# Optimization experiments

Measured on AMD Instinct MI355X. Metric: run time of the kernel, lower is better.

The kernel has to match this reference:

```python
import jax, jax.numpy as jnp
import numpy as np

EPS = 1e-12  # matches torch F.normalize eps


def setup_inputs() -> dict:
    key = jax.random.key(0)
    k_x, k_w, k_b, k_c, k_f = jax.random.split(key, 5)
    N, C, H, W = 32, 128, 64, 64
    K = 64
    x = jax.random.normal(k_x, (N, C, H, W), dtype=jnp.float32)
    conv_w = jax.random.normal(k_w, (K, C), dtype=jnp.float32) * 0.05  # 1x1 conv weight [K,C,1,1] squeezed
    conv_b = jax.random.normal(k_b, (K,), dtype=jnp.float32) * 0.05
    centroids = jax.random.uniform(k_c, (K, C), dtype=jnp.float32)
    fc_w = jax.random.normal(k_f, (1, K), dtype=jnp.float32) * 0.1  # nn.Linear(K,1,bias=False).weight
    return {"x": x, "conv_w": conv_w, "conv_b": conv_b, "centroids": centroids, "fc_w": fc_w}


def _l2norm(v, axis):
    return v / jnp.maximum(jnp.linalg.norm(v, axis=axis, keepdims=True), EPS)


def reference(x, conv_w, conv_b, centroids, fc_w):
    N, C, H, W = x.shape
    K = conv_w.shape[0]
    # descriptor-wise L2 normalize over channel dim
    x = _l2norm(x, axis=1)
    xf = x.reshape(N, C, H * W)                                   # [N,C,S]
    # 1x1 conv == per-pixel linear over channels
    logits = jnp.einsum('kc,ncs->nks', conv_w, xf) + conv_b[None, :, None]
    a = jax.nn.softmax(logits, axis=1)                            # [N,K,S] soft assignment
    # VLAD: sum_s a[n,k,s] * (x[n,:,s] - centroids[k,:]), loop-free
    vlad = jnp.einsum('nks,ncs->nkc', a, xf) \
           - a.sum(axis=-1)[..., None] * centroids[None, :, :]    # [N,K,C]
    # intra-normalization over descriptor dim
    vlad = _l2norm(vlad, axis=2)
    # lastfc: [N,C,K] @ [K] -> [N,C]
    out = jnp.einsum('nkc,k->nc', vlad, fc_w[0])
    return out
```

## Files before the change

### kernel.cpp

```cpp
#include <hip/hip_runtime.h>
#include <math.h>

#define Nn 32
#define Cc 128
#define Ss 4096
#define Kk 64
#define NCHUNK 16
#define SCHUNK (Ss / NCHUNK)
#define ST 64
#define NSUB (SCHUNK / ST)
#define BLK 256

#define XCS 72
#define XTS 136
#define LKS 68
#define AS  72
#define RS  17

typedef __attribute__((ext_vector_type(8))) short short8;
typedef __attribute__((ext_vector_type(4))) float float4v;

__device__ __forceinline__ unsigned f2bf(float f) {
    unsigned u = __builtin_bit_cast(unsigned, f);
    return (u + 0x7fffu + ((u >> 16) & 1u)) >> 16;
}
__device__ __forceinline__ unsigned pack2(float a, float b) {
    return f2bf(a) | (f2bf(b) << 16);
}

__global__ __launch_bounds__(BLK, 2) void netvlad_main(
    const float* __restrict__ x,
    const float* __restrict__ conv_w,
    const float* __restrict__ conv_b,
    float* __restrict__ vlad,
    float* __restrict__ asum)
{
    __shared__ __align__(16) unsigned short xC[Cc * XCS];
    __shared__ __align__(16) float Lbuf[ST * LKS];
    __shared__ __align__(16) unsigned short aB[Kk * AS];
    __shared__ float red[ST * RS];
    __shared__ float invn[ST];
    unsigned short* xT = (unsigned short*)Lbuf;

    const int t    = threadIdx.x;
    const int n    = blockIdx.y;
    const int w    = t >> 6;
    const int l    = t & 63;
    const int m    = l & 15;
    const int quad = l >> 4;
    const int p    = t >> 2;
    const int ii   = t & 3;

    short8 wfrag[4];
    {
        const float* wr_ = conv_w + (16 * w + m) * Cc;
#pragma unroll
        for (int ks = 0; ks < 4; ++ks) {
            float4 wa = *(const float4*)(wr_ + 32 * ks + 8 * quad);
            float4 wb = *(const float4*)(wr_ + 32 * ks + 8 * quad + 4);
            union { short8 s8; unsigned u[4]; } W_;
            W_.u[0] = pack2(wa.x, wa.y);
            W_.u[1] = pack2(wa.z, wa.w);
            W_.u[2] = pack2(wb.x, wb.y);
            W_.u[3] = pack2(wb.z, wb.w);
            wfrag[ks] = W_.s8;
        }
    }
    float bias_r[4];
#pragma unroll
    for (int r = 0; r < 4; ++r) bias_r[r] = conv_b[16 * w + 4 * quad + r];

    float4v acc[8];
#pragma unroll
    for (int nt = 0; nt < 8; ++nt) acc[nt] = (float4v){0.f, 0.f, 0.f, 0.f};
    float asum_part[16];
#pragma unroll
    for (int j = 0; j < 16; ++j) asum_part[j] = 0.f;

    const float* xn = x + (size_t)n * Cc * Ss;

    for (int sub = 0; sub < NSUB; ++sub) {
        const int s0 = blockIdx.x * SCHUNK + sub * ST;
        __syncthreads();

        {
            float sp0 = 0.f, sp1 = 0.f, sp2 = 0.f, sp3 = 0.f;
            const int sq = (t & 15) << 2;
#pragma unroll
            for (int r = 0; r < 8; ++r) {
                int c = (t >> 4) + 16 * r;
                float4 v = *(const float4*)(xn + (size_t)c * Ss + s0 + sq);
                sp0 += v.x * v.x; sp1 += v.y * v.y;
                sp2 += v.z * v.z; sp3 += v.w * v.w;
                uint2 pk = make_uint2(pack2(v.x, v.y), pack2(v.z, v.w));
                *(uint2*)&xC[c * XCS + sq] = pk;
            }
            red[(sq + 0) * RS + (t >> 4)] = sp0;
            red[(sq + 1) * RS + (t >> 4)] = sp1;
            red[(sq + 2) * RS + (t >> 4)] = sp2;
            red[(sq + 3) * RS + (t >> 4)] = sp3;
        }
        __syncthreads();

        if (t < ST) {
            float tot = 0.f;
#pragma unroll
            for (int i = 0; i < 16; ++i) tot += red[t * RS + i];
            invn[t] = 1.0f / fmaxf(sqrtf(tot), 1e-12f);
        }
        {
            int s = t & 63, oct0 = t >> 6;
#pragma unroll
            for (int q = 0; q < 4; ++q) {
                int oct = oct0 + 4 * q;
                uint4 dd;
                dd.x = (unsigned)xC[(8 * oct + 0) * XCS + s] | ((unsigned)xC[(8 * oct + 1) * XCS + s] << 16);
                dd.y = (unsigned)xC[(8 * oct + 2) * XCS + s] | ((unsigned)xC[(8 * oct + 3) * XCS + s] << 16);
                dd.z = (unsigned)xC[(8 * oct + 4) * XCS + s] | ((unsigned)xC[(8 * oct + 5) * XCS + s] << 16);
                dd.w = (unsigned)xC[(8 * oct + 6) * XCS + s] | ((unsigned)xC[(8 * oct + 7) * XCS + s] << 16);
                *(uint4*)&xT[s * XTS + 8 * oct] = dd;
            }
        }
        __syncthreads();

        float4v Lr[4];
#pragma unroll
        for (int nt = 0; nt < 4; ++nt) Lr[nt] = (float4v){0.f, 0.f, 0.f, 0.f};
#pragma unroll
        for (int nt = 0; nt < 4; ++nt) {
#pragma unroll
            for (int ks = 0; ks < 4; ++ks) {
                short8 b = *(const short8*)&xT[(16 * nt + m) * XTS + 32 * ks + 8 * quad];
                Lr[nt] = __builtin_amdgcn_mfma_f32_16x16x32_bf16(wfrag[ks], b, Lr[nt], 0, 0, 0);
            }
        }
        __syncthreads();

#pragma unroll
        for (int nt = 0; nt < 4; ++nt) {
            float iv = invn[16 * nt + m];
            float4 o;
            o.x = Lr[nt].x * iv + bias_r[0];
            o.y = Lr[nt].y * iv + bias_r[1];
            o.z = Lr[nt].z * iv + bias_r[2];
            o.w = Lr[nt].w * iv + bias_r[3];
            *(float4*)&Lbuf[(16 * nt + m) * LKS + 16 * w + 4 * quad] = o;
        }
        __syncthreads();

        {
            float lv[16];
#pragma unroll
            for (int j = 0; j < 16; ++j) lv[j] = Lbuf[p * LKS + ii + 4 * j];
            float mx = lv[0];
#pragma unroll
            for (int j = 1; j < 16; ++j) mx = fmaxf(mx, lv[j]);
            mx = fmaxf(mx, __shfl_xor(mx, 1));
            mx = fmaxf(mx, __shfl_xor(mx, 2));
            float e[16];
            float lsum = 0.f;
#pragma unroll
            for (int j = 0; j < 16; ++j) { e[j] = __expf(lv[j] - mx); lsum += e[j]; }
            lsum += __shfl_xor(lsum, 1);
            lsum += __shfl_xor(lsum, 2);
            float itot = 1.0f / lsum;
            float sca  = itot * invn[p];
#pragma unroll
            for (int j = 0; j < 16; ++j) {
                float av = e[j] * itot;
                asum_part[j] += av;
                aB[(ii + 4 * j) * AS + p] = (unsigned short)f2bf(e[j] * sca);
            }
        }
        __syncthreads();

#pragma unroll
        for (int ks = 0; ks < 2; ++ks) {
            short8 af = *(const short8*)&aB[(16 * w + m) * AS + 32 * ks + 8 * quad];
#pragma unroll
            for (int nt = 0; nt < 8; ++nt) {
                short8 bf_ = *(const short8*)&xC[(16 * nt + m) * XCS + 32 * ks + 8 * quad];
                acc[nt] = __builtin_amdgcn_mfma_f32_16x16x32_bf16(af, bf_, acc[nt], 0, 0, 0);
            }
        }
    }

    float* vb = vlad + ((size_t)n * Kk + 16 * w + 4 * quad) * Cc + m;
#pragma unroll
    for (int nt = 0; nt < 8; ++nt) {
        atomicAdd(vb + 0 * Cc + 16 * nt, acc[nt].x);
        atomicAdd(vb + 1 * Cc + 16 * nt, acc[nt].y);
        atomicAdd(vb + 2 * Cc + 16 * nt, acc[nt].z);
        atomicAdd(vb + 3 * Cc + 16 * nt, acc[nt].w);
    }

    __syncthreads();
#pragma unroll
    for (int j = 0; j < 16; ++j) Lbuf[p * LKS + ii + 4 * j] = asum_part[j];
    __syncthreads();
    if (t < Kk) {
        float s_ = 0.f;
        for (int p2 = 0; p2 < ST; ++p2) s_ += Lbuf[p2 * LKS + t];
        atomicAdd(&asum[n * Kk + t], s_);
    }
}

__global__ __launch_bounds__(256) void netvlad_final(
    const float* __restrict__ vlad, const float* __restrict__ asum,
    const float* __restrict__ centroids, const float* __restrict__ fc_w,
    float* __restrict__ out)
{
    __shared__ float scale_s[Kk];
    __shared__ float asum_s[Kk];
    __shared__ float red2[Kk][4];

    const int n = blockIdx.x;
    const int t = threadIdx.x;
    const int k = t >> 2;
    const int q = t & 3;

    const float* vr = vlad + ((size_t)n * Kk + k) * Cc + q * 32;
    const float* cr = centroids + k * Cc + q * 32;
    const float  as = asum[n * Kk + k];

    float ssq = 0.f;
#pragma unroll
    for (int i = 0; i < 8; ++i) {
        float4 v4 = *(const float4*)(vr + 4 * i);
        float4 c4 = *(const float4*)(cr + 4 * i);
        float d0 = v4.x - as * c4.x;
        float d1 = v4.y - as * c4.y;
        float d2 = v4.z - as * c4.z;
        float d3 = v4.w - as * c4.w;
        ssq += d0 * d0 + d1 * d1 + d2 * d2 + d3 * d3;
    }
    red2[k][q] = ssq;
    __syncthreads();
    if (q == 0) {
        float tot = red2[k][0] + red2[k][1] + red2[k][2] + red2[k][3];
        scale_s[k] = fc_w[k] / fmaxf(sqrtf(tot), 1e-12f);
        asum_s[k]  = as;
    }
    __syncthreads();

    if (t < Cc) {
        const int c = t;
        const float* vbp = vlad + (size_t)n * Kk * Cc + c;
        float o = 0.f;
#pragma unroll 8
        for (int k2 = 0; k2 < Kk; ++k2)
            o += scale_s[k2] * (vbp[k2 * Cc] - asum_s[k2] * centroids[k2 * Cc + c]);
        out[n * Cc + c] = o;
    }
}

extern "C" void kernel_launch(void* const* d_in, const int* in_sizes, int n_in,
                              void* d_out, int out_size, void* d_ws, size_t ws_size,
                              hipStream_t stream) {
    (void)in_sizes; (void)n_in; (void)out_size; (void)ws_size;
    const float* x         = (const float*)d_in[0];
    const float* conv_w    = (const float*)d_in[1];
    const float* conv_b    = (const float*)d_in[2];
    const float* centroids = (const float*)d_in[3];
    const float* fc_w      = (const float*)d_in[4];
    float* out = (float*)d_out;

    float* vlad = (float*)d_ws;
    float* asum = vlad + (size_t)Nn * Kk * Cc;
    size_t zero_bytes = ((size_t)Nn * Kk * Cc + (size_t)Nn * Kk) * sizeof(float);
    hipMemsetAsync(d_ws, 0, zero_bytes, stream);

    dim3 grid(NCHUNK, Nn);
    netvlad_main<<<grid, BLK, 0, stream>>>(x, conv_w, conv_b, vlad, asum);
    netvlad_final<<<Nn, 256, 0, stream>>>(vlad, asum, centroids, fc_w, out);
}
```

Before: 119.3 us.

## Keep conv logits in registers and do softmax per wave without LDS round trip

Each wave now computes all 64 clusters for its own 16 pixels, holding all four weight k-tiles in registers. The softmax is then done directly on the MFMA accumulators with cross-lane shuffles, which removes the Lbuf spill and two barriers per subtile. It also adds a faster transpose using 32-bit LDS reads, computes the per-pixel norm with shuffles, and reduces asum with shuffles. NCHUNK is doubled and the occupancy hint is raised to 3, at the cost of more weight registers and more atomics.

```diff
diff --git a/kernel.cpp b/kernel.cpp
--- a/kernel.cpp
+++ b/kernel.cpp
@@ -5,7 +5,7 @@
 #define Cc 128
 #define Ss 4096
 #define Kk 64
-#define NCHUNK 16
+#define NCHUNK 32
 #define SCHUNK (Ss / NCHUNK)
 #define ST 64
 #define NSUB (SCHUNK / ST)
@@ -13,9 +13,8 @@
 
 #define XCS 72
 #define XTS 136
-#define LKS 68
 #define AS  72
-#define RS  17
+#define RSS 68
 
 typedef __attribute__((ext_vector_type(8))) short short8;
 typedef __attribute__((ext_vector_type(4))) float float4v;
@@ -28,7 +27,7 @@
     return f2bf(a) | (f2bf(b) << 16);
 }
 
-__global__ __launch_bounds__(BLK, 2) void netvlad_main(
+__global__ __launch_bounds__(BLK, 3) void netvlad_main(
     const float* __restrict__ x,
     const float* __restrict__ conv_w,
     const float* __restrict__ conv_b,
@@ -36,24 +35,25 @@
     float* __restrict__ asum)
 {
     __shared__ __align__(16) unsigned short xC[Cc * XCS];
-    __shared__ __align__(16) float Lbuf[ST * LKS];
+    __shared__ __align__(16) unsigned short xT[ST * XTS];
     __shared__ __align__(16) unsigned short aB[Kk * AS];
-    __shared__ float red[ST * RS];
-    __shared__ float invn[ST];
-    unsigned short* xT = (unsigned short*)Lbuf;
+    __shared__ __align__(16) float red[16 * RSS];
+    __shared__ float bias_lds[Kk];
+    float* asumLDS = red;
 
     const int t    = threadIdx.x;
     const int n    = blockIdx.y;
     const int w    = t >> 6;
-    const int l    = t & 63;
-    const int m    = l & 15;
-    const int quad = l >> 4;
-    const int p    = t >> 2;
-    const int ii   = t & 3;
-
-    short8 wfrag[4];
-    {
-        const float* wr_ = conv_w + (16 * w + m) * Cc;
+    const int m    = t & 15;
+    const int quad = (t >> 4) & 3;
+    const int sw   = 16 * w + m;
+
+    if (t < Kk) bias_lds[t] = conv_b[t];
+
+    short8 wfrag[4][4];
+#pragma unroll
+    for (int kt = 0; kt < 4; ++kt) {
+        const float* wr_ = conv_w + (16 * kt + m) * Cc;
 #pragma unroll
         for (int ks = 0; ks < 4; ++ks) {
             float4 wa = *(const float4*)(wr_ + 32 * ks + 8 * quad);
@@ -63,12 +63,9 @@
             W_.u[1] = pack2(wa.z, wa.w);
             W_.u[2] = pack2(wb.x, wb.y);
             W_.u[3] = pack2(wb.z, wb.w);
-            wfrag[ks] = W_.s8;
-        }
-    }
-    float bias_r[4];
-#pragma unroll
-    for (int r = 0; r < 4; ++r) bias_r[r] = conv_b[16 * w + 4 * quad + r];
+            wfrag[kt][ks] = W_.s8;
+        }
+    }
 
     float4v acc[8];
 #pragma unroll
@@ -84,92 +81,90 @@
         __syncthreads();
 
         {
+            const int g  = t >> 4;
+            const int sq = (t & 15) << 2;
             float sp0 = 0.f, sp1 = 0.f, sp2 = 0.f, sp3 = 0.f;
-            const int sq = (t & 15) << 2;
 #pragma unroll
             for (int r = 0; r < 8; ++r) {
-                int c = (t >> 4) + 16 * r;
+                int c = g + 16 * r;
                 float4 v = *(const float4*)(xn + (size_t)c * Ss + s0 + sq);
                 sp0 += v.x * v.x; sp1 += v.y * v.y;
                 sp2 += v.z * v.z; sp3 += v.w * v.w;
                 uint2 pk = make_uint2(pack2(v.x, v.y), pack2(v.z, v.w));
                 *(uint2*)&xC[c * XCS + sq] = pk;
             }
-            red[(sq + 0) * RS + (t >> 4)] = sp0;
-            red[(sq + 1) * RS + (t >> 4)] = sp1;
-            red[(sq + 2) * RS + (t >> 4)] = sp2;
-            red[(sq + 3) * RS + (t >> 4)] = sp3;
-        }
-        __syncthreads();
-
-        if (t < ST) {
-            float tot = 0.f;
-#pragma unroll
-            for (int i = 0; i < 16; ++i) tot += red[t * RS + i];
-            invn[t] = 1.0f / fmaxf(sqrtf(tot), 1e-12f);
-        }
+            *(float4*)&red[g * RSS + sq] = make_float4(sp0, sp1, sp2, sp3);
+        }
+        __syncthreads();
+
+#pragma unroll
+        for (int pass = 0; pass < 2; ++pass) {
+            int oct = (t >> 5) + 8 * pass;
+            int sp2_ = t & 31;
+            unsigned r_[8];
+#pragma unroll
+            for (int j = 0; j < 8; ++j)
+                r_[j] = *(const unsigned*)&xC[(8 * oct + j) * XCS + 2 * sp2_];
+            uint4 lo, hi;
+            lo.x = (r_[0] & 0xffffu) | (r_[1] << 16);
+            lo.y = (r_[2] & 0xffffu) | (r_[3] << 16);
+            lo.z = (r_[4] & 0xffffu) | (r_[5] << 16);
+            lo.w = (r_[6] & 0xffffu) | (r_[7] << 16);
+            hi.x = (r_[0] >> 16) | (r_[1] & 0xffff0000u);
+            hi.y = (r_[2] >> 16) | (r_[3] & 0xffff0000u);
+            hi.z = (r_[4] >> 16) | (r_[5] & 0xffff0000u);
+            hi.w = (r_[6] >> 16) | (r_[7] & 0xffff0000u);
+            *(uint4*)&xT[(2 * sp2_ + 0) * XTS + 8 * oct] = lo;
+            *(uint4*)&xT[(2 * sp2_ + 1) * XTS + 8 * oct] = hi;
+        }
+
+        float pr = red[(4 * quad + 0) * RSS + sw] + red[(4 * quad + 1) * RSS + sw]
+                 + red[(4 * quad + 2) * RSS + sw] + red[(4 * quad + 3) * RSS + sw];
+        pr += __shfl_xor(pr, 16);
+        pr += __shfl_xor(pr, 32);
+        float invn = 1.0f / fmaxf(sqrtf(pr), 1e-12f);
+        __syncthreads();
+
+        float4v Lr[4];
+#pragma unroll
+        for (int kt = 0; kt < 4; ++kt) Lr[kt] = (float4v){0.f, 0.f, 0.f, 0.f};
+#pragma unroll
+        for (int ks = 0; ks < 4; ++ks) {
+            short8 b = *(const short8*)&xT[sw * XTS + 32 * ks + 8 * quad];
+#pragma unroll
+            for (int kt = 0; kt < 4; ++kt)
+                Lr[kt] = __builtin_amdgcn_mfma_f32_16x16x32_bf16(wfrag[kt][ks], b, Lr[kt], 0, 0, 0);
+        }
+
         {
-            int s = t & 63, oct0 = t >> 6;
-#pragma unroll
-            for (int q = 0; q < 4; ++q) {
-                int oct = oct0 + 4 * q;
-                uint4 dd;
-                dd.x = (unsigned)xC[(8 * oct + 0) * XCS + s] | ((unsigned)xC[(8 * oct + 1) * XCS + s] << 16);
-                dd.y = (unsigned)xC[(8 * oct + 2) * XCS + s] | ((unsigned)xC[(8 * oct + 3) * XCS + s] << 16);
-                dd.z = (unsigned)xC[(8 * oct + 4) * XCS + s] | ((unsigned)xC[(8 * oct + 5) * XCS + s] << 16);
-                dd.w = (unsigned)xC[(8 * oct + 6) * XCS + s] | ((unsigned)xC[(8 * oct + 7) * XCS + s] << 16);
-                *(uint4*)&xT[s * XTS + 8 * oct] = dd;
-            }
-        }
-        __syncthreads();
-
-        float4v Lr[4];
-#pragma unroll
-        for (int nt = 0; nt < 4; ++nt) Lr[nt] = (float4v){0.f, 0.f, 0.f, 0.f};
-#pragma unroll
-        for (int nt = 0; nt < 4; ++nt) {
-#pragma unroll
-            for (int ks = 0; ks < 4; ++ks) {
-                short8 b = *(const short8*)&xT[(16 * nt + m) * XTS + 32 * ks + 8 * quad];
-                Lr[nt] = __builtin_amdgcn_mfma_f32_16x16x32_bf16(wfrag[ks], b, Lr[nt], 0, 0, 0);
-            }
-        }
-        __syncthreads();
-
-#pragma unroll
-        for (int nt = 0; nt < 4; ++nt) {
-            float iv = invn[16 * nt + m];
-            float4 o;
-            o.x = Lr[nt].x * iv + bias_r[0];
-            o.y = Lr[nt].y * iv + bias_r[1];
-            o.z = Lr[nt].z * iv + bias_r[2];
-            o.w = Lr[nt].w * iv + bias_r[3];
-            *(float4*)&Lbuf[(16 * nt + m) * LKS + 16 * w + 4 * quad] = o;
-        }
-        __syncthreads();
-
-        {
-            float lv[16];
-#pragma unroll
-            for (int j = 0; j < 16; ++j) lv[j] = Lbuf[p * LKS + ii + 4 * j];
-            float mx = lv[0];
-#pragma unroll
-            for (int j = 1; j < 16; ++j) mx = fmaxf(mx, lv[j]);
-            mx = fmaxf(mx, __shfl_xor(mx, 1));
-            mx = fmaxf(mx, __shfl_xor(mx, 2));
-            float e[16];
+            float lg[16];
+#pragma unroll
+            for (int kt = 0; kt < 4; ++kt) {
+                lg[4 * kt + 0] = Lr[kt].x * invn + bias_lds[16 * kt + 4 * quad + 0];
+                lg[4 * kt + 1] = Lr[kt].y * invn + bias_lds[16 * kt + 4 * quad + 1];
+                lg[4 * kt + 2] = Lr[kt].z * invn + bias_lds[16 * kt + 4 * quad + 2];
+                lg[4 * kt + 3] = Lr[kt].w * invn + bias_lds[16 * kt + 4 * quad + 3];
+            }
+            float mx = lg[0];
+#pragma unroll
+            for (int j = 1; j < 16; ++j) mx = fmaxf(mx, lg[j]);
+            mx = fmaxf(mx, __shfl_xor(mx, 16));
+            mx = fmaxf(mx, __shfl_xor(mx, 32));
             float lsum = 0.f;
 #pragma unroll
-            for (int j = 0; j < 16; ++j) { e[j] = __expf(lv[j] - mx); lsum += e[j]; }
-            lsum += __shfl_xor(lsum, 1);
-            lsum += __shfl_xor(lsum, 2);
+            for (int j = 0; j < 16; ++j) { lg[j] = __expf(lg[j] - mx); lsum += lg[j]; }
+            lsum += __shfl_xor(lsum, 16);
+            lsum += __shfl_xor(lsum, 32);
             float itot = 1.0f / lsum;
-            float sca  = itot * invn[p];
-#pragma unroll
-            for (int j = 0; j < 16; ++j) {
-                float av = e[j] * itot;
-                asum_part[j] += av;
-                aB[(ii + 4 * j) * AS + p] = (unsigned short)f2bf(e[j] * sca);
+            float sca  = itot * invn;
+#pragma unroll
+            for (int j = 0; j < 16; ++j) asum_part[j] += lg[j] * itot;
+#pragma unroll
+            for (int kt = 0; kt < 4; ++kt) {
+                aB[(16 * kt + 4 * quad + 0) * AS + sw] = (unsigned short)f2bf(lg[4 * kt + 0] * sca);
+                aB[(16 * kt + 4 * quad + 1) * AS + sw] = (unsigned short)f2bf(lg[4 * kt + 1] * sca);
+                aB[(16 * kt + 4 * quad + 2) * AS + sw] = (unsigned short)f2bf(lg[4 * kt + 2] * sca);
+                aB[(16 * kt + 4 * quad + 3) * AS + sw] = (unsigned short)f2bf(lg[4 * kt + 3] * sca);
             }
         }
         __syncthreads();
@@ -194,13 +189,26 @@
         atomicAdd(vb + 3 * Cc + 16 * nt, acc[nt].w);
     }
 
-    __syncthreads();
-#pragma unroll
-    for (int j = 0; j < 16; ++j) Lbuf[p * LKS + ii + 4 * j] = asum_part[j];
+#pragma unroll
+    for (int j = 0; j < 16; ++j) {
+        float v = asum_part[j];
+        v += __shfl_xor(v, 1);
+        v += __shfl_xor(v, 2);
+        v += __shfl_xor(v, 4);
+        v += __shfl_xor(v, 8);
+        asum_part[j] = v;
+    }
+    __syncthreads();
+    if (m == 0) {
+#pragma unroll
+        for (int kt = 0; kt < 4; ++kt)
+#pragma unroll
+            for (int r = 0; r < 4; ++r)
+                asumLDS[w * 64 + 16 * kt + 4 * quad + r] = asum_part[4 * kt + r];
+    }
     __syncthreads();
     if (t < Kk) {
-        float s_ = 0.f;
-        for (int p2 = 0; p2 < ST; ++p2) s_ += Lbuf[p2 * LKS + t];
+        float s_ = asumLDS[t] + asumLDS[64 + t] + asumLDS[128 + t] + asumLDS[192 + t];
         atomicAdd(&asum[n * Kk + t], s_);
     }
 }
```

After: 148.7 us. 1.25x slower.
